# Optimization experiments

Hardware: AMD Instinct MI355X
Metric: run time of the kernel (lower is better)

Reference implementation:

```python
import jax, jax.numpy as jnp
import numpy as np

NEG_MIN = jnp.finfo(jnp.float32).min


def setup_inputs() -> dict:
    key = jax.random.key(0)
    kq, kk, kv, km = jax.random.split(key, 4)
    B, H, S, D = 2, 16, 2048, 64
    return {
        "query": jax.random.normal(kq, (B, H, S, D), dtype=jnp.float32),
        "key": jax.random.normal(kk, (B, H, S, D), dtype=jnp.float32),
        "value": jax.random.normal(kv, (B, H, S, D), dtype=jnp.float32),
        "attention_mask": jax.random.randint(km, (B, S), 0, 2, dtype=jnp.int32),
    }


def reference(query, key, value, attention_mask):
    # query/key/value: [B, H, S, D]; attention_mask: [B, S] (1 = keep, 0 = pad)
    D = query.shape[-1]
    scores = jnp.einsum("bhqd,bhkd->bhqk", query, key) / jnp.sqrt(jnp.float32(D))
    # 2-D mask branch: (1 - mask) * finfo.min added as additive bias
    pad = (1.0 - attention_mask.astype(jnp.float32))[:, None, None, :] * NEG_MIN
    scores = scores + pad
    # softmax in fp32 (scale_attention_softmax_in_fp32=True), cast back to query dtype
    probs = jax.nn.softmax(scores.astype(jnp.float32), axis=-1).astype(query.dtype)
    # attention_dropout = 0.0 -> no dropout
    out = jnp.einsum("bhqk,bhkd->bhqd", probs, value)
    return out
```

## Files before the change

kernel.cpp:

```cpp
#include <hip/hip_runtime.h>

typedef __attribute__((ext_vector_type(8))) short short8;
typedef __attribute__((ext_vector_type(16))) float f32x16;
typedef __attribute__((ext_vector_type(4))) int int4v;

#define LOG2E 1.4426950408889634f

#if __has_builtin(__builtin_amdgcn_exp2f)
#define EXP2(x) __builtin_amdgcn_exp2f(x)
#else
#define EXP2(x) exp2f(x)
#endif

__device__ __forceinline__ unsigned cvtpk(float lo, float hi) {
    unsigned r;
    asm("v_cvt_pk_bf16_f32 %0, %1, %2" : "=v"(r) : "v"(lo), "v"(hi));
    return r;
}

__global__ __launch_bounds__(256) void attn_fwd(
    const float* __restrict__ Q, const float* __restrict__ K,
    const float* __restrict__ V, const int* __restrict__ M,
    float* __restrict__ O)
{
    constexpr int S = 2048, D = 64, KVB = 64;
    __shared__ unsigned short k_lds[KVB * D];
    __shared__ unsigned short vt_lds[D * KVB];
    __shared__ float bias_lds[S];
    __shared__ float l_buf[4][32];

    const int t = threadIdx.x;
    const int lane = t & 63, wid = t >> 6;
    const int l31 = lane & 31, hi = lane >> 5;

    const int lin = blockIdx.x;
    const int wgid = (lin & 7) * 64 + (lin >> 3);
    const int bh = wgid >> 4;
    const int qblk = wgid & 15;
    const int b = bh >> 4;

    const int* mrow = M + b * S;
    for (int i = t; i < S; i += 256)
        bias_lds[i] = mrow[i] ? -24.0f : -__builtin_inff();

    const int qrow0 = qblk * 128 + wid * 32;
    const float* qp = Q + ((size_t)bh * S + qrow0 + l31) * D;
    const float qs = 0.125f * LOG2E;
    short8 qf[4];
    #pragma unroll
    for (int c = 0; c < 4; ++c) {
        const float* p = qp + c * 16 + hi * 8;
        float4 x = *(const float4*)p;
        float4 y = *(const float4*)(p + 4);
        int4v w = { (int)cvtpk(x.x * qs, x.y * qs), (int)cvtpk(x.z * qs, x.w * qs),
                    (int)cvtpk(y.x * qs, y.y * qs), (int)cvtpk(y.z * qs, y.w * qs) };
        qf[c] = __builtin_bit_cast(short8, w);
    }

    f32x16 acc0 = {0,0,0,0,0,0,0,0,0,0,0,0,0,0,0,0};
    f32x16 acc1 = {0,0,0,0,0,0,0,0,0,0,0,0,0,0,0,0};
    float l = 0.0f;

    const int skey = t >> 2, sds2 = (t & 3) * 32;
    const int swzk = (skey & 7) << 4;
    const int vkey2 = lane * 2;
    const int vds = wid * 16;

    const int krow0 = l31 * 128;
    const int krow1 = (32 + l31) * 128;
    const int kx = (hi * 16) ^ ((l31 & 7) << 4);
    const int vrow0 = l31 * 128;
    const int vrow1 = (32 + l31) * 128;

    const float* kbase = K + (size_t)bh * S * D;
    const float* vbase = V + (size_t)bh * S * D;

    for (int kt = 0; kt < S; kt += KVB) {
        {
            const float* kp = kbase + (size_t)(kt + skey) * D + (t & 3) * 16;
            float4 a0 = ((const float4*)kp)[0];
            float4 a1 = ((const float4*)kp)[1];
            float4 a2 = ((const float4*)kp)[2];
            float4 a3 = ((const float4*)kp)[3];
            int4v w0 = { (int)cvtpk(a0.x,a0.y), (int)cvtpk(a0.z,a0.w),
                         (int)cvtpk(a1.x,a1.y), (int)cvtpk(a1.z,a1.w) };
            int4v w1 = { (int)cvtpk(a2.x,a2.y), (int)cvtpk(a2.z,a2.w),
                         (int)cvtpk(a3.x,a3.y), (int)cvtpk(a3.z,a3.w) };
            *(int4v*)((char*)k_lds + skey * 128 + (sds2 ^ swzk)) = w0;
            *(int4v*)((char*)k_lds + skey * 128 + ((sds2 + 16) ^ swzk)) = w1;

            const float* vp = vbase + (size_t)(kt + lane) * D + vds;
            float4 b0 = ((const float4*)vp)[0];
            float4 b1 = ((const float4*)vp)[1];
            float4 b2 = ((const float4*)vp)[2];
            float4 b3 = ((const float4*)vp)[3];
            unsigned cc[8] = { cvtpk(b0.x,b0.y), cvtpk(b0.z,b0.w),
                               cvtpk(b1.x,b1.y), cvtpk(b1.z,b1.w),
                               cvtpk(b2.x,b2.y), cvtpk(b2.z,b2.w),
                               cvtpk(b3.x,b3.y), cvtpk(b3.z,b3.w) };
            #pragma unroll
            for (int i = 0; i < 16; ++i) {
                int row = vds + i;
                int byte_off = row * 128 + (vkey2 ^ ((row & 7) << 4));
                unsigned val = (i & 1) ? (cc[i >> 1] >> 16) : (cc[i >> 1] & 0xffffu);
                *(unsigned short*)((char*)vt_lds + byte_off) = (unsigned short)val;
            }
        }
        __syncthreads();

        f32x16 s0 = {0,0,0,0,0,0,0,0,0,0,0,0,0,0,0,0};
        f32x16 s1 = {0,0,0,0,0,0,0,0,0,0,0,0,0,0,0,0};
        #pragma unroll
        for (int c = 0; c < 4; ++c) {
            short8 ka = *(const short8*)((char*)k_lds + krow0 + (kx ^ (c << 5)));
            short8 kb = *(const short8*)((char*)k_lds + krow1 + (kx ^ (c << 5)));
            s0 = __builtin_amdgcn_mfma_f32_32x32x16_bf16(ka, qf[c], s0, 0, 0, 0);
            s1 = __builtin_amdgcn_mfma_f32_32x32x16_bf16(kb, qf[c], s1, 0, 0, 0);
        }

        float rs = 0.0f;
        #pragma unroll
        for (int rg = 0; rg < 4; ++rg) {
            float4 bz0 = *(const float4*)&bias_lds[kt + rg * 8 + hi * 4];
            float4 bz1 = *(const float4*)&bias_lds[kt + 32 + rg * 8 + hi * 4];
            const float* z0 = (const float*)&bz0;
            const float* z1 = (const float*)&bz1;
            #pragma unroll
            for (int j = 0; j < 4; ++j) {
                int r = rg * 4 + j;
                float e0 = EXP2(s0[r] + z0[j]);
                float e1 = EXP2(s1[r] + z1[j]);
                s0[r] = e0; s1[r] = e1;
                rs += e0 + e1;
            }
        }
        rs += __shfl_xor(rs, 32);
        l += rs;

        short8 pw[4];
        #pragma unroll
        for (int w = 0; w < 4; ++w) {
            int r0 = (w & 1) * 8;
            float q0 = (w >> 1) ? s1[r0+0] : s0[r0+0];
            float q1 = (w >> 1) ? s1[r0+1] : s0[r0+1];
            float q2 = (w >> 1) ? s1[r0+2] : s0[r0+2];
            float q3 = (w >> 1) ? s1[r0+3] : s0[r0+3];
            float q4 = (w >> 1) ? s1[r0+4] : s0[r0+4];
            float q5 = (w >> 1) ? s1[r0+5] : s0[r0+5];
            float q6 = (w >> 1) ? s1[r0+6] : s0[r0+6];
            float q7 = (w >> 1) ? s1[r0+7] : s0[r0+7];
            unsigned x0 = cvtpk(q0, q1);
            unsigned x1 = cvtpk(q2, q3);
            unsigned x2 = cvtpk(q4, q5);
            unsigned x3 = cvtpk(q6, q7);
            unsigned sx0 = (unsigned)__shfl_xor((int)x0, 32);
            unsigned sx1 = (unsigned)__shfl_xor((int)x1, 32);
            unsigned sx2 = (unsigned)__shfl_xor((int)x2, 32);
            unsigned sx3 = (unsigned)__shfl_xor((int)x3, 32);
            int4v wv = { (int)(hi ? sx2 : x0),
                         (int)(hi ? sx3 : x1),
                         (int)(hi ? x2 : sx0),
                         (int)(hi ? x3 : sx1) };
            pw[w] = __builtin_bit_cast(short8, wv);
        }

        #pragma unroll
        for (int w = 0; w < 4; ++w) {
            short8 vf0 = *(const short8*)((char*)vt_lds + vrow0 + (kx ^ (w << 5)));
            short8 vf1 = *(const short8*)((char*)vt_lds + vrow1 + (kx ^ (w << 5)));
            acc0 = __builtin_amdgcn_mfma_f32_32x32x16_bf16(pw[w], vf0, acc0, 0, 0, 0);
            acc1 = __builtin_amdgcn_mfma_f32_32x32x16_bf16(pw[w], vf1, acc1, 0, 0, 0);
        }
        __syncthreads();
    }

    if (hi == 0) l_buf[wid][l31] = 1.0f / l;
    __syncthreads();

    float* ob = O + ((size_t)bh * S + qrow0) * D;
    #pragma unroll
    for (int rg = 0; rg < 4; ++rg) {
        float4 invl = *(const float4*)&l_buf[wid][rg * 8 + hi * 4];
        const float* iv = (const float*)&invl;
        #pragma unroll
        for (int j = 0; j < 4; ++j) {
            int r = rg * 4 + j;
            int qr = rg * 8 + hi * 4 + j;
            ob[qr * 64 + l31] = acc0[r] * iv[j];
            ob[qr * 64 + 32 + l31] = acc1[r] * iv[j];
        }
    }
}

extern "C" void kernel_launch(void* const* d_in, const int* in_sizes, int n_in,
                              void* d_out, int out_size, void* d_ws, size_t ws_size,
                              hipStream_t stream) {
    const float* Q = (const float*)d_in[0];
    const float* K = (const float*)d_in[1];
    const float* V = (const float*)d_in[2];
    const int*   M = (const int*)d_in[3];
    float* O = (float*)d_out;
    attn_fwd<<<dim3(512), dim3(256), 0, stream>>>(Q, K, V, M, O);
}
```

Baseline: 162.8 us.

## Double-buffer K/V tiles in LDS with register prefetch and MFMA priority

Turns the single-buffered K/V LDS staging into a two-slot ping-pong. The next tile's global loads are issued into registers before the current tile's compute, and they are converted and written into the alternate LDS slot after the PV MFMAs. This removes one barrier per iteration and hides global load latency behind the MFMA and softmax work. It also raises wave priority around the MFMA blocks and splits the row-sum reduction into partial sums. The cost is double the K/V LDS footprint and higher register pressure from the prefetched float4s, which may reduce occupancy.

```diff
diff --git a/kernel.cpp b/kernel.cpp
--- a/kernel.cpp
+++ b/kernel.cpp
@@ -23,9 +23,9 @@
     const float* __restrict__ V, const int* __restrict__ M,
     float* __restrict__ O)
 {
-    constexpr int S = 2048, D = 64, KVB = 64;
-    __shared__ unsigned short k_lds[KVB * D];
-    __shared__ unsigned short vt_lds[D * KVB];
+    constexpr int S = 2048, D = 64, KVB = 64, NT = S / KVB;
+    __shared__ unsigned short k_lds[2][KVB * D];
+    __shared__ unsigned short vt_lds[2][D * KVB];
     __shared__ float bias_lds[S];
     __shared__ float l_buf[4][32];
 
@@ -63,6 +63,7 @@
 
     const int skey = t >> 2, sds2 = (t & 3) * 32;
     const int swzk = (skey & 7) << 4;
+    const int kwb = skey * 128;
     const int vkey2 = lane * 2;
     const int vds = wid * 16;
 
@@ -72,68 +73,84 @@
     const int vrow0 = l31 * 128;
     const int vrow1 = (32 + l31) * 128;
 
-    const float* kbase = K + (size_t)bh * S * D;
-    const float* vbase = V + (size_t)bh * S * D;
-
-    for (int kt = 0; kt < S; kt += KVB) {
-        {
-            const float* kp = kbase + (size_t)(kt + skey) * D + (t & 3) * 16;
-            float4 a0 = ((const float4*)kp)[0];
-            float4 a1 = ((const float4*)kp)[1];
-            float4 a2 = ((const float4*)kp)[2];
-            float4 a3 = ((const float4*)kp)[3];
-            int4v w0 = { (int)cvtpk(a0.x,a0.y), (int)cvtpk(a0.z,a0.w),
-                         (int)cvtpk(a1.x,a1.y), (int)cvtpk(a1.z,a1.w) };
-            int4v w1 = { (int)cvtpk(a2.x,a2.y), (int)cvtpk(a2.z,a2.w),
-                         (int)cvtpk(a3.x,a3.y), (int)cvtpk(a3.z,a3.w) };
-            *(int4v*)((char*)k_lds + skey * 128 + (sds2 ^ swzk)) = w0;
-            *(int4v*)((char*)k_lds + skey * 128 + ((sds2 + 16) ^ swzk)) = w1;
-
-            const float* vp = vbase + (size_t)(kt + lane) * D + vds;
-            float4 b0 = ((const float4*)vp)[0];
-            float4 b1 = ((const float4*)vp)[1];
-            float4 b2 = ((const float4*)vp)[2];
-            float4 b3 = ((const float4*)vp)[3];
-            unsigned cc[8] = { cvtpk(b0.x,b0.y), cvtpk(b0.z,b0.w),
-                               cvtpk(b1.x,b1.y), cvtpk(b1.z,b1.w),
-                               cvtpk(b2.x,b2.y), cvtpk(b2.z,b2.w),
-                               cvtpk(b3.x,b3.y), cvtpk(b3.z,b3.w) };
-            #pragma unroll
-            for (int i = 0; i < 16; ++i) {
-                int row = vds + i;
-                int byte_off = row * 128 + (vkey2 ^ ((row & 7) << 4));
-                unsigned val = (i & 1) ? (cc[i >> 1] >> 16) : (cc[i >> 1] & 0xffffu);
-                *(unsigned short*)((char*)vt_lds + byte_off) = (unsigned short)val;
-            }
-        }
-        __syncthreads();
+    const float* kpt = K + (size_t)bh * S * D + (size_t)skey * D + (t & 3) * 16;
+    const float* vpt = V + (size_t)bh * S * D + (size_t)lane * D + vds;
+
+    float4 ka0, ka1, ka2, ka3, vb0, vb1, vb2, vb3;
+
+    auto load_tile = [&]() {
+        ka0 = ((const float4*)kpt)[0]; ka1 = ((const float4*)kpt)[1];
+        ka2 = ((const float4*)kpt)[2]; ka3 = ((const float4*)kpt)[3];
+        vb0 = ((const float4*)vpt)[0]; vb1 = ((const float4*)vpt)[1];
+        vb2 = ((const float4*)vpt)[2]; vb3 = ((const float4*)vpt)[3];
+        kpt += KVB * D; vpt += KVB * D;
+    };
+    auto write_tile = [&](unsigned short* kdst, unsigned short* vdst) {
+        int4v w0 = { (int)cvtpk(ka0.x,ka0.y), (int)cvtpk(ka0.z,ka0.w),
+                     (int)cvtpk(ka1.x,ka1.y), (int)cvtpk(ka1.z,ka1.w) };
+        int4v w1 = { (int)cvtpk(ka2.x,ka2.y), (int)cvtpk(ka2.z,ka2.w),
+                     (int)cvtpk(ka3.x,ka3.y), (int)cvtpk(ka3.z,ka3.w) };
+        *(int4v*)((char*)kdst + kwb + (sds2 ^ swzk)) = w0;
+        *(int4v*)((char*)kdst + kwb + ((sds2 + 16) ^ swzk)) = w1;
+        unsigned cc[8] = { cvtpk(vb0.x,vb0.y), cvtpk(vb0.z,vb0.w),
+                           cvtpk(vb1.x,vb1.y), cvtpk(vb1.z,vb1.w),
+                           cvtpk(vb2.x,vb2.y), cvtpk(vb2.z,vb2.w),
+                           cvtpk(vb3.x,vb3.y), cvtpk(vb3.z,vb3.w) };
+        #pragma unroll
+        for (int i = 0; i < 16; ++i) {
+            int row = vds + i;
+            int off = row * 128 + (vkey2 ^ ((row & 7) << 4));
+            unsigned val = (i & 1) ? (cc[i >> 1] >> 16) : (cc[i >> 1] & 0xffffu);
+            *(unsigned short*)((char*)vdst + off) = (unsigned short)val;
+        }
+    };
+
+    load_tile();
+    write_tile(k_lds[0], vt_lds[0]);
+    __syncthreads();
+
+    #pragma unroll 2
+    for (int it = 0; it < NT; ++it) {
+        const int cur = it & 1;
+        const bool more = (it + 1 < NT);
+        if (more) load_tile();
+
+        const char* kc = (const char*)k_lds[cur];
+        const char* vc = (const char*)vt_lds[cur];
+        const int ktoff = it * KVB;
 
         f32x16 s0 = {0,0,0,0,0,0,0,0,0,0,0,0,0,0,0,0};
         f32x16 s1 = {0,0,0,0,0,0,0,0,0,0,0,0,0,0,0,0};
+        __builtin_amdgcn_s_setprio(1);
         #pragma unroll
         for (int c = 0; c < 4; ++c) {
-            short8 ka = *(const short8*)((char*)k_lds + krow0 + (kx ^ (c << 5)));
-            short8 kb = *(const short8*)((char*)k_lds + krow1 + (kx ^ (c << 5)));
-            s0 = __builtin_amdgcn_mfma_f32_32x32x16_bf16(ka, qf[c], s0, 0, 0, 0);
-            s1 = __builtin_amdgcn_mfma_f32_32x32x16_bf16(kb, qf[c], s1, 0, 0, 0);
-        }
-
-        float rs = 0.0f;
+            short8 kaf = *(const short8*)(kc + krow0 + (kx ^ (c << 5)));
+            short8 kbf = *(const short8*)(kc + krow1 + (kx ^ (c << 5)));
+            s0 = __builtin_amdgcn_mfma_f32_32x32x16_bf16(kaf, qf[c], s0, 0, 0, 0);
+            s1 = __builtin_amdgcn_mfma_f32_32x32x16_bf16(kbf, qf[c], s1, 0, 0, 0);
+        }
+        __builtin_amdgcn_s_setprio(0);
+
+        float rsp0 = 0.0f, rsp1 = 0.0f, rsp2 = 0.0f, rsp3 = 0.0f;
         #pragma unroll
         for (int rg = 0; rg < 4; ++rg) {
-            float4 bz0 = *(const float4*)&bias_lds[kt + rg * 8 + hi * 4];
-            float4 bz1 = *(const float4*)&bias_lds[kt + 32 + rg * 8 + hi * 4];
+            float4 bz0 = *(const float4*)&bias_lds[ktoff + rg * 8 + hi * 4];
+            float4 bz1 = *(const float4*)&bias_lds[ktoff + 32 + rg * 8 + hi * 4];
             const float* z0 = (const float*)&bz0;
             const float* z1 = (const float*)&bz1;
+            float rp = 0.0f;
             #pragma unroll
             for (int j = 0; j < 4; ++j) {
                 int r = rg * 4 + j;
                 float e0 = EXP2(s0[r] + z0[j]);
                 float e1 = EXP2(s1[r] + z1[j]);
                 s0[r] = e0; s1[r] = e1;
-                rs += e0 + e1;
+                rp += e0 + e1;
             }
-        }
+            if (rg == 0) rsp0 = rp; else if (rg == 1) rsp1 = rp;
+            else if (rg == 2) rsp2 = rp; else rsp3 = rp;
+        }
+        float rs = (rsp0 + rsp1) + (rsp2 + rsp3);
         rs += __shfl_xor(rs, 32);
         l += rs;
 
@@ -164,13 +181,17 @@
             pw[w] = __builtin_bit_cast(short8, wv);
         }
 
+        __builtin_amdgcn_s_setprio(1);
         #pragma unroll
         for (int w = 0; w < 4; ++w) {
-            short8 vf0 = *(const short8*)((char*)vt_lds + vrow0 + (kx ^ (w << 5)));
-            short8 vf1 = *(const short8*)((char*)vt_lds + vrow1 + (kx ^ (w << 5)));
+            short8 vf0 = *(const short8*)(vc + vrow0 + (kx ^ (w << 5)));
+            short8 vf1 = *(const short8*)(vc + vrow1 + (kx ^ (w << 5)));
             acc0 = __builtin_amdgcn_mfma_f32_32x32x16_bf16(pw[w], vf0, acc0, 0, 0, 0);
             acc1 = __builtin_amdgcn_mfma_f32_32x32x16_bf16(pw[w], vf1, acc1, 0, 0, 0);
         }
+        __builtin_amdgcn_s_setprio(0);
+
+        if (more) write_tile(k_lds[cur ^ 1], vt_lds[cur ^ 1]);
         __syncthreads();
     }
 
```

Result: faster. 153.1 us (-6.0%).
